# Kernel tuning notes

Hardware: AMD Instinct MI355X
Metric: run time of the kernel (lower is better)

The kernel has to match this reference:

```python
import jax, jax.numpy as jnp
import numpy as np

B, S, D = 2, 2048, 2048
H, KV, HD = 32, 8, 64
REP = H // KV  # 4


def setup_inputs() -> dict:
    key = jax.random.key(0)
    ks = jax.random.split(key, 5)
    x = jax.random.normal(ks[0], (B, S, D), jnp.float32)
    # Llama rope frequencies: theta=10000, pairs of adjacent dims
    inv_freq = 1.0 / (10000.0 ** (np.arange(0, HD, 2, dtype=np.float64) / HD))  # [HD/2]
    ang = np.outer(np.arange(S, dtype=np.float64), inv_freq)  # [S, HD/2]
    freqs_cis = jnp.asarray(np.stack([np.cos(ang), np.sin(ang)], axis=-1), jnp.float32)  # [S, HD/2, 2]
    wq = jax.random.normal(ks[1], (H * HD, D), jnp.float32) * 0.02
    wk = jax.random.normal(ks[2], (KV * HD, D), jnp.float32) * 0.02
    wv = jax.random.normal(ks[3], (KV * HD, D), jnp.float32) * 0.02
    wo = jax.random.normal(ks[4], (D, H * HD), jnp.float32) * 0.02
    return {"x": x, "freqs_cis": freqs_cis, "wq": wq, "wk": wk, "wv": wv, "wo": wo}


def _apply_rope(t, cos, sin):
    # t: [B,S,nh,HD]; cos/sin: [S,HD/2]; complex multiply on adjacent pairs
    b, s, nh, hd = t.shape
    t2 = t.reshape(b, s, nh, hd // 2, 2)
    tr, ti = t2[..., 0], t2[..., 1]
    c = cos[None, :, None, :]
    sn = sin[None, :, None, :]
    out = jnp.stack([tr * c - ti * sn, tr * sn + ti * c], axis=-1)
    return out.reshape(b, s, nh, hd)


def reference(x, freqs_cis, wq, wk, wv, wo):
    # QKV projections (torch Linear: y = x @ W.T)
    q = jnp.einsum('bsd,ed->bse', x, wq).reshape(B, S, H, HD)
    k = jnp.einsum('bsd,ed->bse', x, wk).reshape(B, S, KV, HD)
    v = jnp.einsum('bsd,ed->bse', x, wv).reshape(B, S, KV, HD)
    cos, sin = freqs_cis[..., 0], freqs_cis[..., 1]
    q = _apply_rope(q, cos, sin)
    k = _apply_rope(k, cos, sin)
    # GQA without materializing repeated K/V: group query heads by KV head
    qg = q.reshape(B, S, KV, REP, HD)
    scale = 1.0 / jnp.sqrt(jnp.asarray(HD, q.dtype))
    scores = jnp.einsum('bsgrd,btgd->bgrst', qg, k) * scale  # [B,KV,REP,S,S]
    causal = jnp.tril(jnp.ones((S, S), bool))
    scores = jnp.where(causal, scores, -jnp.inf)
    p = jax.nn.softmax(scores, axis=-1)
    o = jnp.einsum('bgrst,btgd->bsgrd', p, v).reshape(B, S, H * HD)
    return jnp.einsum('bse,de->bsd', o, wo)
```

## Files before the change

kernel.cpp:

```cpp
#include <hip/hip_runtime.h>
#include <cstdint>
#include <cstddef>

#define B_ 2
#define S_ 2048
#define D_ 2048
#define H_ 32
#define KV_ 8
#define HD_ 64
#define M_ (B_*S_)
#define EQ_ (H_*HD_)
#define EK_ (KV_*HD_)

typedef unsigned short u16;
typedef __attribute__((ext_vector_type(8))) short s16x8;
typedef __attribute__((ext_vector_type(4))) float f32x4;

#define QSCALE 0.18033688011112042f
#define EXPOFF 15.869645449778564f

#if __has_builtin(__builtin_amdgcn_exp2f)
#define EXP2(x) __builtin_amdgcn_exp2f(x)
#else
#define EXP2(x) __expf((x) * 0.6931471805599453f)
#endif

__device__ __forceinline__ u16 f2bf(float f) {
  unsigned u = __float_as_uint(f);
  u += 0x7fffu + ((u >> 16) & 1u);
  return (u16)(u >> 16);
}
__device__ __forceinline__ unsigned pk2(float a, float b) {
  unsigned ua = __float_as_uint(a) + 0x8000u;
  unsigned ub = __float_as_uint(b) + 0x8000u;
  return __builtin_amdgcn_perm(ub, ua, 0x07060302);
}
__device__ __forceinline__ f32x4 mfma16(s16x8 a, s16x8 b, f32x4 c) {
  return __builtin_amdgcn_mfma_f32_16x16x32_bf16(a, b, c, 0, 0, 0);
}
__device__ __forceinline__ void gl_lds16(const void* g, void* l) {
  __builtin_amdgcn_global_load_lds(
      (const __attribute__((address_space(1))) void*)g,
      (__attribute__((address_space(3))) void*)l, 16, 0, 0);
}

__global__ void cast_all(const float4* __restrict__ x, const float4* __restrict__ wq,
                         const float4* __restrict__ wk, const float4* __restrict__ wv,
                         const float4* __restrict__ wo, ushort4* __restrict__ dst) {
  int i = blockIdx.x * 256 + threadIdx.x;
  const float4* src; int off;
  if (i < 2097152)      { src = x;  off = i; }
  else if (i < 3145728) { src = wq; off = i - 2097152; }
  else if (i < 3407872) { src = wk; off = i - 3145728; }
  else if (i < 3670016) { src = wv; off = i - 3407872; }
  else                  { src = wo; off = i - 3670016; }
  float4 v = src[off];
  ushort4 r;
  r.x = f2bf(v.x); r.y = f2bf(v.y); r.z = f2bf(v.z); r.w = f2bf(v.w);
  dst[i] = r;
}

__global__ __launch_bounds__(256)
void gemm_qkv(const u16* __restrict__ A, const u16* __restrict__ Bw,
              u16* __restrict__ qb, u16* __restrict__ kb, u16* __restrict__ vtb,
              const float* __restrict__ fc) {
  __shared__ __align__(16) u16 As[2][128 * 32];
  __shared__ __align__(16) u16 Bs[2][96 * 32];
  const int tid  = threadIdx.x;
  const int lane = tid & 63;
  const int wave = tid >> 6;
  const int m0 = blockIdx.y * 128;
  const int n0 = blockIdx.x * 96;
  const int wm = (wave >> 1) * 64;
  const int wn = (wave & 1) * 48;
  const int l15 = lane & 15;
  const int quad = lane >> 4;

  const int ca0 = tid,      ra0 = ca0 >> 2, pa0 = ca0 & 3;
  const int ca1 = tid + 256, ra1 = ca1 >> 2, pa1 = ca1 & 3;
  const int cb0 = tid,      rb0 = cb0 >> 2, pb0 = cb0 & 3;
  const int cb1 = tid + 256, rb1 = cb1 >> 2, pb1 = cb1 & 3;
  const u16* Ap0 = A + (size_t)(m0 + ra0) * D_ + (pa0 ^ ((ra0 >> 1) & 3)) * 8;
  const u16* Ap1 = A + (size_t)(m0 + ra1) * D_ + (pa1 ^ ((ra1 >> 1) & 3)) * 8;
  const u16* Bp0 = Bw + (size_t)(n0 + rb0) * D_ + (pb0 ^ ((rb0 >> 1) & 3)) * 8;
  const u16* Bp1 = Bw + (size_t)(n0 + rb1) * D_ + (pb1 ^ ((rb1 >> 1) & 3)) * 8;
  const bool doB1 = (tid < 128);

  f32x4 acc[4][3] = {};

  gl_lds16(Ap0, &As[0][ca0 * 8]);
  gl_lds16(Ap1, &As[0][ca1 * 8]);
  gl_lds16(Bp0, &Bs[0][cb0 * 8]);
  if (doB1) gl_lds16(Bp1, &Bs[0][cb1 * 8]);
  __syncthreads();

  for (int ks = 0; ks < 64; ++ks) {
    if (ks + 1 < 64) {
      const int nb = (ks + 1) & 1;
      const int ko = (ks + 1) * 32;
      gl_lds16(Ap0 + ko, &As[nb][ca0 * 8]);
      gl_lds16(Ap1 + ko, &As[nb][ca1 * 8]);
      gl_lds16(Bp0 + ko, &Bs[nb][cb0 * 8]);
      if (doB1) gl_lds16(Bp1 + ko, &Bs[nb][cb1 * 8]);
    }

    const u16* as = &As[ks & 1][0];
    const u16* bs = &Bs[ks & 1][0];
    s16x8 af[4], bfr[3];
    #pragma unroll
    for (int mi = 0; mi < 4; ++mi) {
      int row = wm + mi * 16 + l15;
      af[mi] = *(const s16x8*)&as[row * 32 + (quad ^ ((row >> 1) & 3)) * 8];
    }
    #pragma unroll
    for (int ni = 0; ni < 3; ++ni) {
      int row = wn + ni * 16 + l15;
      bfr[ni] = *(const s16x8*)&bs[row * 32 + (quad ^ ((row >> 1) & 3)) * 8];
    }
    #pragma unroll
    for (int mi = 0; mi < 4; ++mi)
      #pragma unroll
      for (int ni = 0; ni < 3; ++ni)
        acc[mi][ni] = mfma16(af[mi], bfr[ni], acc[mi][ni]);

    __syncthreads();
  }

  const float sg = (l15 & 1) ? 1.f : -1.f;
  #pragma unroll
  for (int mi = 0; mi < 4; ++mi) {
    #pragma unroll
    for (int ni = 0; ni < 3; ++ni) {
      const int col = n0 + wn + ni * 16 + l15;
      if (col < 2560) {
        const bool isQ = (col < 2048);
        u16* dst = isQ ? qb : kb;
        const int ncol0 = isQ ? 0 : 2048;
        const int ndim  = isQ ? EQ_ : EK_;
        const float scale = isQ ? QSCALE : 1.0f;
        const int ip = (col & 63) >> 1;
        #pragma unroll
        for (int r = 0; r < 4; ++r) {
          int row = m0 + wm + mi * 16 + quad * 4 + r;
          const float* fr = fc + (size_t)(row & (S_ - 1)) * 64;
          float c  = fr[ip * 2];
          float sn = fr[ip * 2 + 1];
          float v = acc[mi][ni][r];
          float p = __shfl_xor(v, 1, 64);
          float o = (v * c + sg * (p * sn)) * scale;
          dst[(size_t)row * ndim + col - ncol0] = f2bf(o);
        }
      } else {
        const int vcol = col - 2560;
        uint2 w;
        w.x = pk2(acc[mi][ni][0], acc[mi][ni][1]);
        w.y = pk2(acc[mi][ni][2], acc[mi][ni][3]);
        *(uint2*)(vtb + (size_t)vcol * M_ + m0 + wm + mi * 16 + quad * 4) = w;
      }
    }
  }
}

__global__ __launch_bounds__(256)
void gemm_o(const u16* __restrict__ A, const u16* __restrict__ Bw, float* __restrict__ C,
            int Ndim, int Kdim) {
  __shared__ __align__(16) u16 As[2][64 * 32];
  __shared__ __align__(16) u16 Bs[2][128 * 32];
  const int tid  = threadIdx.x;
  const int lane = tid & 63;
  const int wave = tid >> 6;
  const int m0 = blockIdx.y * 64;
  const int n0 = blockIdx.x * 128;
  const int wm = (wave >> 1) * 32;
  const int wn = (wave & 1) * 64;
  const int l15 = lane & 15;
  const int quad = lane >> 4;

  const int ca0 = tid,      ra0 = ca0 >> 2, pa0 = ca0 & 3;
  const int cb0 = tid,      rb0 = cb0 >> 2, pb0 = cb0 & 3;
  const int cb1 = tid + 256, rb1 = cb1 >> 2, pb1 = cb1 & 3;
  const u16* Ap0 = A + (size_t)(m0 + ra0) * Kdim + (pa0 ^ ((ra0 >> 1) & 3)) * 8;
  const u16* Bp0 = Bw + (size_t)(n0 + rb0) * Kdim + (pb0 ^ ((rb0 >> 1) & 3)) * 8;
  const u16* Bp1 = Bw + (size_t)(n0 + rb1) * Kdim + (pb1 ^ ((rb1 >> 1) & 3)) * 8;

  f32x4 acc[2][4] = {};

  const int nsteps = Kdim >> 5;

  gl_lds16(Ap0, &As[0][ca0 * 8]);
  gl_lds16(Bp0, &Bs[0][cb0 * 8]);
  gl_lds16(Bp1, &Bs[0][cb1 * 8]);
  __syncthreads();

  for (int ks = 0; ks < nsteps; ++ks) {
    if (ks + 1 < nsteps) {
      const int nb = (ks + 1) & 1;
      const int ko = (ks + 1) * 32;
      gl_lds16(Ap0 + ko, &As[nb][ca0 * 8]);
      gl_lds16(Bp0 + ko, &Bs[nb][cb0 * 8]);
      gl_lds16(Bp1 + ko, &Bs[nb][cb1 * 8]);
    }

    const u16* as = &As[ks & 1][0];
    const u16* bs = &Bs[ks & 1][0];
    s16x8 af[2], bfr[4];
    #pragma unroll
    for (int mi = 0; mi < 2; ++mi) {
      int row = wm + mi * 16 + l15;
      af[mi] = *(const s16x8*)&as[row * 32 + (quad ^ ((row >> 1) & 3)) * 8];
    }
    #pragma unroll
    for (int ni = 0; ni < 4; ++ni) {
      int row = wn + ni * 16 + l15;
      bfr[ni] = *(const s16x8*)&bs[row * 32 + (quad ^ ((row >> 1) & 3)) * 8];
    }
    #pragma unroll
    for (int mi = 0; mi < 2; ++mi)
      #pragma unroll
      for (int ni = 0; ni < 4; ++ni)
        acc[mi][ni] = mfma16(af[mi], bfr[ni], acc[mi][ni]);

    __syncthreads();
  }

  #pragma unroll
  for (int mi = 0; mi < 2; ++mi) {
    #pragma unroll
    for (int r = 0; r < 4; ++r) {
      int row = m0 + wm + mi * 16 + quad * 4 + r;
      size_t base = (size_t)row * Ndim + n0 + wn;
      #pragma unroll
      for (int ni = 0; ni < 4; ++ni)
        C[base + ni * 16 + l15] = acc[mi][ni][r];
    }
  }
}

__device__ __forceinline__ void qk_pass(const s16x8* kk0, const s16x8* kk1,
                                        s16x8 q0, s16x8 q1, bool msk, int rowX,
                                        int t0, int quad, float& sum,
                                        s16x8& p0v, s16x8& p1v) {
  union PU { s16x8 v; unsigned u[4]; };
  f32x4 sS[4];
  #pragma unroll
  for (int ts = 0; ts < 4; ++ts) {
    f32x4 s = {};
    s = mfma16(kk0[ts], q0, s);
    s = mfma16(kk1[ts], q1, s);
    sS[ts] = s;
  }
  if (msk) {
    #pragma unroll
    for (int ts = 0; ts < 4; ++ts) {
      const int tb = t0 + ((ts & 2) << 4) + ((ts & 1) << 2) + quad * 8;
      #pragma unroll
      for (int r = 0; r < 4; ++r) if (tb + r > rowX) sS[ts][r] = -1e30f;
    }
  }
  float e[16];
  #pragma unroll
  for (int ts = 0; ts < 4; ++ts)
    #pragma unroll
    for (int r = 0; r < 4; ++r) {
      float x = EXP2(sS[ts][r] - EXPOFF);
      e[ts * 4 + r] = x;
      sum += x;
    }
  PU p0u, p1u;
  p0u.u[0] = pk2(e[0],  e[1]);  p0u.u[1] = pk2(e[2],  e[3]);
  p0u.u[2] = pk2(e[4],  e[5]);  p0u.u[3] = pk2(e[6],  e[7]);
  p1u.u[0] = pk2(e[8],  e[9]);  p1u.u[1] = pk2(e[10], e[11]);
  p1u.u[2] = pk2(e[12], e[13]); p1u.u[3] = pk2(e[14], e[15]);
  p0v = p0u.v; p1v = p1u.v;
}

__global__ __launch_bounds__(256, 2)
void flash_attn(const u16* __restrict__ qb, const u16* __restrict__ kb,
                const u16* __restrict__ vtb, u16* __restrict__ ob) {
  const int bx = blockIdx.x;
  const int hy = blockIdx.y;
  const int b  = blockIdx.z;
  const int h0 = hy * 2;
  const int g  = hy >> 1;
  const int tid  = threadIdx.x;
  const int lane = tid & 63;
  const int wave = tid >> 6;
  const int l15  = lane & 15;
  const int quad = lane >> 4;
  const int kq   = quad * 8;

  const int Tlo = bx, Thi = 31 - bx;
  const int n_lo = Tlo + 1, n_hi = Thi + 1;
  const int rL = Tlo * 64 + wave * 16;
  const int rH = Thi * 64 + wave * 16;
  const int rowL = rL + l15;
  const int rowH = rH + l15;

  __shared__ __align__(16) u16 Ks[2][8 * 512];
  __shared__ __align__(16) u16 Vs[2][8 * 512];

  const u16* qpH0 = qb + (size_t)(b * S_ + rH + l15) * EQ_ + h0 * HD_;
  const u16* qpL0 = qb + (size_t)(b * S_ + rL + l15) * EQ_ + h0 * HD_;
  s16x8 qHa0 = *(const s16x8*)(qpH0 + kq);
  s16x8 qHa1 = *(const s16x8*)(qpH0 + 32 + kq);
  s16x8 qHb0 = *(const s16x8*)(qpH0 + HD_ + kq);
  s16x8 qHb1 = *(const s16x8*)(qpH0 + HD_ + 32 + kq);
  s16x8 qLa0 = *(const s16x8*)(qpL0 + kq);
  s16x8 qLa1 = *(const s16x8*)(qpL0 + 32 + kq);
  s16x8 qLb0 = *(const s16x8*)(qpL0 + HD_ + kq);
  s16x8 qLb1 = *(const s16x8*)(qpL0 + HD_ + 32 + kq);

  f32x4 OHa[4] = {}, OHb[4] = {}, OLa[4] = {}, OLb[4] = {};
  float sumHa = 0.f, sumHb = 0.f, sumLa = 0.f, sumLb = 0.f;

  const int sw = wave & 1;
  const bool doK = (wave < 2);

  const int tl = (lane & 0x23) | ((lane & 0x0C) << 1) | ((lane & 0x10) >> 2);

  const u16* stbase;
  size_t     tstride;
  if (doK) {
    stbase  = kb + (size_t)(b * S_ + tl) * EK_ + g * HD_ + sw * 32;
    tstride = (size_t)64 * EK_;
  } else {
    stbase  = vtb + (size_t)(g * HD_ + lane) * M_ + b * S_ + sw * 32;
    tstride = 64;
  }
  const int ldoff = sw * 4 * 512 + lane * 8;
  u16* mybuf0 = (doK ? &Ks[0][0] : &Vs[0][0]) + ldoff;
  u16* mybuf1 = (doK ? &Ks[1][0] : &Vs[1][0]) + ldoff;

  #pragma unroll
  for (int r = 0; r < 4; ++r)
    gl_lds16(stbase + r * 8, mybuf0 + r * 512);
  __syncthreads();

  for (int kt = 0; kt < n_hi; ++kt) {
    const int t0 = kt * 64;
    const u16* kcur = &Ks[kt & 1][0];
    const u16* vcur = &Vs[kt & 1][0];

    if (kt + 1 < n_hi) {
      const u16* src = stbase + (size_t)(kt + 1) * tstride;
      u16* dst = ((kt + 1) & 1) ? mybuf1 : mybuf0;
      #pragma unroll
      for (int r = 0; r < 4; ++r)
        gl_lds16(src + r * 8, dst + r * 512);
    }

    const bool do_lo = (kt < n_lo);
    const bool mH = (kt == n_hi - 1);
    const bool mL = (kt == n_lo - 1);

    s16x8 kk0[4], kk1[4];
    #pragma unroll
    for (int ts = 0; ts < 4; ++ts) {
      kk0[ts] = *(const s16x8*)&kcur[quad * 512 + (ts * 16 + l15) * 8];
      kk1[ts] = *(const s16x8*)&kcur[(4 + quad) * 512 + (ts * 16 + l15) * 8];
    }

    s16x8 pHa0, pHa1, pHb0, pHb1, pLa0, pLa1, pLb0, pLb1;
    qk_pass(kk0, kk1, qHa0, qHa1, mH, rowH, t0, quad, sumHa, pHa0, pHa1);
    qk_pass(kk0, kk1, qHb0, qHb1, mH, rowH, t0, quad, sumHb, pHb0, pHb1);
    if (do_lo) {
      qk_pass(kk0, kk1, qLa0, qLa1, mL, rowL, t0, quad, sumLa, pLa0, pLa1);
      qk_pass(kk0, kk1, qLb0, qLb1, mL, rowL, t0, quad, sumLb, pLb0, pLb1);
    } else {
      pLa0 = s16x8{}; pLa1 = s16x8{}; pLb0 = s16x8{}; pLb1 = s16x8{};
    }

    #pragma unroll
    for (int df = 0; df < 4; ++df) {
      s16x8 v0 = *(const s16x8*)&vcur[quad * 512 + (df * 16 + l15) * 8];
      s16x8 v1 = *(const s16x8*)&vcur[(4 + quad) * 512 + (df * 16 + l15) * 8];
      OHa[df] = mfma16(v1, pHa1, mfma16(v0, pHa0, OHa[df]));
      OHb[df] = mfma16(v1, pHb1, mfma16(v0, pHb0, OHb[df]));
      if (do_lo) {
        OLa[df] = mfma16(v1, pLa1, mfma16(v0, pLa0, OLa[df]));
        OLb[df] = mfma16(v1, pLb1, mfma16(v0, pLb0, OLb[df]));
      }
    }

    __syncthreads();
  }

  sumHa += __shfl_xor(sumHa, 16, 64); sumHa += __shfl_xor(sumHa, 32, 64);
  sumHb += __shfl_xor(sumHb, 16, 64); sumHb += __shfl_xor(sumHb, 32, 64);
  sumLa += __shfl_xor(sumLa, 16, 64); sumLa += __shfl_xor(sumLa, 32, 64);
  sumLb += __shfl_xor(sumLb, 16, 64); sumLb += __shfl_xor(sumLb, 32, 64);
  float iHa = 1.f / sumHa, iHb = 1.f / sumHb;
  float iLa = 1.f / sumLa, iLb = 1.f / sumLb;

  {
    u16* op = ob + (size_t)(b * S_ + rowH) * EQ_ + h0 * HD_;
    #pragma unroll
    for (int df = 0; df < 4; ++df) {
      uint2 w;
      w.x = pk2(OHa[df][0] * iHa, OHa[df][1] * iHa);
      w.y = pk2(OHa[df][2] * iHa, OHa[df][3] * iHa);
      *(uint2*)(op + df * 16 + quad * 4) = w;
      uint2 w2;
      w2.x = pk2(OHb[df][0] * iHb, OHb[df][1] * iHb);
      w2.y = pk2(OHb[df][2] * iHb, OHb[df][3] * iHb);
      *(uint2*)(op + HD_ + df * 16 + quad * 4) = w2;
    }
  }
  {
    u16* op = ob + (size_t)(b * S_ + rowL) * EQ_ + h0 * HD_;
    #pragma unroll
    for (int df = 0; df < 4; ++df) {
      uint2 w;
      w.x = pk2(OLa[df][0] * iLa, OLa[df][1] * iLa);
      w.y = pk2(OLa[df][2] * iLa, OLa[df][3] * iLa);
      *(uint2*)(op + df * 16 + quad * 4) = w;
      uint2 w2;
      w2.x = pk2(OLb[df][0] * iLb, OLb[df][1] * iLb);
      w2.y = pk2(OLb[df][2] * iLb, OLb[df][3] * iLb);
      *(uint2*)(op + HD_ + df * 16 + quad * 4) = w2;
    }
  }
}

extern "C" void kernel_launch(void* const* d_in, const int* in_sizes, int n_in,
                              void* d_out, int out_size, void* d_ws, size_t ws_size,
                              hipStream_t stream) {
  (void)in_sizes; (void)n_in; (void)out_size; (void)ws_size;
  const float* x  = (const float*)d_in[0];
  const float* fc = (const float*)d_in[1];
  const float* wq = (const float*)d_in[2];
  const float* wk = (const float*)d_in[3];
  const float* wv = (const float*)d_in[4];
  const float* wo = (const float*)d_in[5];
  float* out = (float*)d_out;
  char* ws = (char*)d_ws;

  u16* xb  = (u16*)(ws);
  u16* wqb = (u16*)(ws + 16777216);
  u16* wob = (u16*)(ws + 29360128);
  u16* qb  = (u16*)(ws + 37748736);
  u16* kb  = (u16*)(ws + 54525952);
  u16* vtb = (u16*)(ws + 58720256);
  u16* ob  = (u16*)(ws + 62914560);

  cast_all<<<18432, 256, 0, stream>>>((const float4*)x, (const float4*)wq,
                                      (const float4*)wk, (const float4*)wv,
                                      (const float4*)wo, (ushort4*)ws);

  gemm_qkv<<<dim3(32, 32), 256, 0, stream>>>(xb, wqb, qb, kb, vtb, fc);

  flash_attn<<<dim3(16, 16, 2), 256, 0, stream>>>(qb, kb, vtb, ob);

  gemm_o<<<dim3(16, 64), 256, 0, stream>>>(ob, wob, out, D_, EQ_);
}
```

Before: 285.8 us.

## Stage K/V tiles in pairs to halve barriers per attention loop

Each double-buffered LDS stage now holds two 64-key K/V tiles instead of one. The loop walks tile pairs, so one __syncthreads and one prefetch cover two tiles of QK/softmax/PV work. This cuts barrier and loop overhead and gives more compute to hide each prefetch behind. In exchange LDS use doubles to 64KB per block, which may limit occupancy at two blocks per CU, and odd tile counts leave a predicated partial pair.

```diff
diff --git a/kernel.cpp b/kernel.cpp
--- a/kernel.cpp
+++ b/kernel.cpp
@@ -291,13 +291,14 @@
 
   const int Tlo = bx, Thi = 31 - bx;
   const int n_lo = Tlo + 1, n_hi = Thi + 1;
+  const int npair = (n_hi + 1) >> 1;
   const int rL = Tlo * 64 + wave * 16;
   const int rH = Thi * 64 + wave * 16;
   const int rowL = rL + l15;
   const int rowH = rH + l15;
 
-  __shared__ __align__(16) u16 Ks[2][8 * 512];
-  __shared__ __align__(16) u16 Vs[2][8 * 512];
+  __shared__ __align__(16) u16 Ks[2][2][8 * 512];
+  __shared__ __align__(16) u16 Vs[2][2][8 * 512];
 
   const u16* qpH0 = qb + (size_t)(b * S_ + rH + l15) * EQ_ + h0 * HD_;
   const u16* qpL0 = qb + (size_t)(b * S_ + rL + l15) * EQ_ + h0 * HD_;
@@ -319,66 +320,80 @@
   const int tl = (lane & 0x23) | ((lane & 0x0C) << 1) | ((lane & 0x10) >> 2);
 
   const u16* stbase;
-  size_t     tstride;
+  size_t     tsub, tpair;
   if (doK) {
-    stbase  = kb + (size_t)(b * S_ + tl) * EK_ + g * HD_ + sw * 32;
-    tstride = (size_t)64 * EK_;
+    stbase = kb + (size_t)(b * S_ + tl) * EK_ + g * HD_ + sw * 32;
+    tsub   = (size_t)64 * EK_;
+    tpair  = (size_t)128 * EK_;
   } else {
-    stbase  = vtb + (size_t)(g * HD_ + lane) * M_ + b * S_ + sw * 32;
-    tstride = 64;
+    stbase = vtb + (size_t)(g * HD_ + lane) * M_ + b * S_ + sw * 32;
+    tsub   = 64;
+    tpair  = 128;
   }
   const int ldoff = sw * 4 * 512 + lane * 8;
-  u16* mybuf0 = (doK ? &Ks[0][0] : &Vs[0][0]) + ldoff;
-  u16* mybuf1 = (doK ? &Ks[1][0] : &Vs[1][0]) + ldoff;
+  u16* base0 = (doK ? &Ks[0][0][0] : &Vs[0][0][0]) + ldoff;
+  u16* base1 = (doK ? &Ks[1][0][0] : &Vs[1][0][0]) + ldoff;
 
   #pragma unroll
-  for (int r = 0; r < 4; ++r)
-    gl_lds16(stbase + r * 8, mybuf0 + r * 512);
+  for (int st = 0; st < 2; ++st)
+    #pragma unroll
+    for (int r = 0; r < 4; ++r)
+      gl_lds16(stbase + st * tsub + r * 8, base0 + st * 4096 + r * 512);
   __syncthreads();
 
-  for (int kt = 0; kt < n_hi; ++kt) {
-    const int t0 = kt * 64;
-    const u16* kcur = &Ks[kt & 1][0];
-    const u16* vcur = &Vs[kt & 1][0];
-
-    if (kt + 1 < n_hi) {
-      const u16* src = stbase + (size_t)(kt + 1) * tstride;
-      u16* dst = ((kt + 1) & 1) ? mybuf1 : mybuf0;
+  for (int pt = 0; pt < npair; ++pt) {
+    const u16* kcur = &Ks[pt & 1][0][0];
+    const u16* vcur = &Vs[pt & 1][0][0];
+
+    if (pt + 1 < npair) {
+      const u16* src = stbase + (size_t)(pt + 1) * tpair;
+      u16* dst = ((pt + 1) & 1) ? base1 : base0;
       #pragma unroll
-      for (int r = 0; r < 4; ++r)
-        gl_lds16(src + r * 8, dst + r * 512);
-    }
-
-    const bool do_lo = (kt < n_lo);
-    const bool mH = (kt == n_hi - 1);
-    const bool mL = (kt == n_lo - 1);
-
-    s16x8 kk0[4], kk1[4];
-    #pragma unroll
-    for (int ts = 0; ts < 4; ++ts) {
-      kk0[ts] = *(const s16x8*)&kcur[quad * 512 + (ts * 16 + l15) * 8];
-      kk1[ts] = *(const s16x8*)&kcur[(4 + quad) * 512 + (ts * 16 + l15) * 8];
-    }
-
-    s16x8 pHa0, pHa1, pHb0, pHb1, pLa0, pLa1, pLb0, pLb1;
-    qk_pass(kk0, kk1, qHa0, qHa1, mH, rowH, t0, quad, sumHa, pHa0, pHa1);
-    qk_pass(kk0, kk1, qHb0, qHb1, mH, rowH, t0, quad, sumHb, pHb0, pHb1);
-    if (do_lo) {
-      qk_pass(kk0, kk1, qLa0, qLa1, mL, rowL, t0, quad, sumLa, pLa0, pLa1);
-      qk_pass(kk0, kk1, qLb0, qLb1, mL, rowL, t0, quad, sumLb, pLb0, pLb1);
-    } else {
-      pLa0 = s16x8{}; pLa1 = s16x8{}; pLb0 = s16x8{}; pLb1 = s16x8{};
-    }
-
-    #pragma unroll
-    for (int df = 0; df < 4; ++df) {
-      s16x8 v0 = *(const s16x8*)&vcur[quad * 512 + (df * 16 + l15) * 8];
-      s16x8 v1 = *(const s16x8*)&vcur[(4 + quad) * 512 + (df * 16 + l15) * 8];
-      OHa[df] = mfma16(v1, pHa1, mfma16(v0, pHa0, OHa[df]));
-      OHb[df] = mfma16(v1, pHb1, mfma16(v0, pHb0, OHb[df]));
-      if (do_lo) {
-        OLa[df] = mfma16(v1, pLa1, mfma16(v0, pLa0, OLa[df]));
-        OLb[df] = mfma16(v1, pLb1, mfma16(v0, pLb0, OLb[df]));
+      for (int st = 0; st < 2; ++st)
+        #pragma unroll
+        for (int r = 0; r < 4; ++r)
+          gl_lds16(src + st * tsub + r * 8, dst + st * 4096 + r * 512);
+    }
+
+    #pragma unroll 1
+    for (int st = 0; st < 2; ++st) {
+      const int kt = 2 * pt + st;
+      if (kt < n_hi) {
+        const int t0 = kt * 64;
+        const u16* ksub = kcur + st * 4096;
+        const u16* vsub = vcur + st * 4096;
+        const bool do_lo = (kt < n_lo);
+        const bool mH = (kt == n_hi - 1);
+        const bool mL = (kt == n_lo - 1);
+
+        s16x8 kk0[4], kk1[4];
+        #pragma unroll
+        for (int ts = 0; ts < 4; ++ts) {
+          kk0[ts] = *(const s16x8*)&ksub[quad * 512 + (ts * 16 + l15) * 8];
+          kk1[ts] = *(const s16x8*)&ksub[(4 + quad) * 512 + (ts * 16 + l15) * 8];
+        }
+
+        s16x8 pHa0, pHa1, pHb0, pHb1, pLa0, pLa1, pLb0, pLb1;
+        qk_pass(kk0, kk1, qHa0, qHa1, mH, rowH, t0, quad, sumHa, pHa0, pHa1);
+        qk_pass(kk0, kk1, qHb0, qHb1, mH, rowH, t0, quad, sumHb, pHb0, pHb1);
+        if (do_lo) {
+          qk_pass(kk0, kk1, qLa0, qLa1, mL, rowL, t0, quad, sumLa, pLa0, pLa1);
+          qk_pass(kk0, kk1, qLb0, qLb1, mL, rowL, t0, quad, sumLb, pLb0, pLb1);
+        } else {
+          pLa0 = s16x8{}; pLa1 = s16x8{}; pLb0 = s16x8{}; pLb1 = s16x8{};
+        }
+
+        #pragma unroll
+        for (int df = 0; df < 4; ++df) {
+          s16x8 v0 = *(const s16x8*)&vsub[quad * 512 + (df * 16 + l15) * 8];
+          s16x8 v1 = *(const s16x8*)&vsub[(4 + quad) * 512 + (df * 16 + l15) * 8];
+          OHa[df] = mfma16(v1, pHa1, mfma16(v0, pHa0, OHa[df]));
+          OHb[df] = mfma16(v1, pHb1, mfma16(v0, pHb0, OHb[df]));
+          if (do_lo) {
+            OLa[df] = mfma16(v1, pLa1, mfma16(v0, pLa0, OLa[df]));
+            OLb[df] = mfma16(v1, pLb1, mfma16(v0, pLb0, OLb[df]));
+          }
+        }
       }
     }
 
```

New measurement: 294.0 us. +2.9%, slower.
